# Kernel optimization log

Measured on AMD Instinct MI355X. Metric: run time of the kernel, lower is better.

Reference implementation:

```python
import jax, jax.numpy as jnp
import numpy as np

B, S, D = 2, 2048, 2048
H, KVH, HD = 32, 8, 64
GROUPS = H // KVH  # 4
NEG = -1e9


def setup_inputs() -> dict:
    key = jax.random.key(0)
    ks = jax.random.split(key, 5)
    x = jax.random.normal(ks[0], (B, S, D), dtype=jnp.float32)
    # causal additive mask [1,1,S,S]
    causal = jnp.triu(jnp.full((S, S), NEG, dtype=jnp.float32), k=1)[None, None]
    Wq = jax.random.normal(ks[1], (D, D), dtype=jnp.float32) * (D ** -0.5)
    Wk = jax.random.normal(ks[2], (KVH * HD, D), dtype=jnp.float32) * (D ** -0.5)
    Wv = jax.random.normal(ks[3], (KVH * HD, D), dtype=jnp.float32) * (D ** -0.5)
    Wo = jax.random.normal(ks[4], (D, D), dtype=jnp.float32) * (D ** -0.5)
    return {"x": x, "attention_mask": causal, "Wq": Wq, "Wk": Wk, "Wv": Wv, "Wo": Wo}


def reference(x, attention_mask, Wq, Wk, Wv, Wo):
    b, s, _ = x.shape
    # projections (nn.Linear: y = x @ W.T)
    q = (x @ Wq.T).reshape(b, s, H, HD).transpose(0, 2, 1, 3)      # [b,H,s,hd]
    k = (x @ Wk.T).reshape(b, s, KVH, HD).transpose(0, 2, 1, 3)    # [b,KVH,s,hd]
    v = (x @ Wv.T).reshape(b, s, KVH, HD).transpose(0, 2, 1, 3)
    new_kv_cache = (k, v)
    # repeat_interleave over head dim for GQA
    k = jnp.repeat(k, GROUPS, axis=1)  # [b,H,s,hd]
    v = jnp.repeat(v, GROUPS, axis=1)
    scale = 1.0 / jnp.sqrt(jnp.float32(HD))
    scores = jnp.einsum('bhqd,bhkd->bhqk', q, k) * scale
    scores = scores + attention_mask
    attn = jax.nn.softmax(scores.astype(jnp.float32), axis=-1).astype(q.dtype)
    out = jnp.einsum('bhqk,bhkd->bhqd', attn, v)  # [b,H,s,hd]
    out = out.transpose(0, 2, 1, 3).reshape(b, s, H * HD)
    output = out @ Wo.T
    return (output, new_kv_cache[0], new_kv_cache[1])
```

## Files before the change

### kernel.cpp

```cpp
#include <hip/hip_runtime.h>
#include <hip/hip_bf16.h>
#include <stdint.h>

#define B_ 2
#define S_ 2048
#define D_ 2048
#define H_ 32
#define KVH_ 8
#define HD_ 64

typedef __bf16 bf16x8 __attribute__((ext_vector_type(8)));
typedef float f32x4 __attribute__((ext_vector_type(4)));

#define MFMA16(a, b, c) __builtin_amdgcn_mfma_f32_16x16x32_bf16((a), (b), (c), 0, 0, 0)

typedef __attribute__((address_space(1))) void gvoid_t;
typedef __attribute__((address_space(3))) void lvoid_t;

__device__ __forceinline__ void async_ld16(__hip_bfloat16* lds, const __hip_bfloat16* g) {
  __builtin_amdgcn_global_load_lds((gvoid_t*)(void*)(g), (lvoid_t*)(lds), 16, 0, 0);
}

__device__ __forceinline__ unsigned short f2bu(float f) {
  __hip_bfloat16 h = __float2bfloat16(f);
  return *reinterpret_cast<unsigned short*>(&h);
}

__global__ void cast_bf16_kernel(const float* __restrict__ in,
                                 unsigned short* __restrict__ out, int n4) {
  int i = blockIdx.x * blockDim.x + threadIdx.x;
  if (i >= n4) return;
  float4 v = reinterpret_cast<const float4*>(in)[i];
  ushort4 o;
  o.x = f2bu(v.x); o.y = f2bu(v.y); o.z = f2bu(v.z); o.w = f2bu(v.w);
  reinterpret_cast<ushort4*>(out)[i] = o;
}

template <int MODE>
__global__ __launch_bounds__(256, 2)
void gemm_bt(const __hip_bfloat16* __restrict__ A,
             const __hip_bfloat16* __restrict__ W,
             float* __restrict__ Cf, __hip_bfloat16* __restrict__ Cb,
             float* __restrict__ Cf2, __hip_bfloat16* __restrict__ Cb2,
             __hip_bfloat16* __restrict__ Cb3,
             int M, int N, int K) {
  __shared__ __align__(16) __hip_bfloat16 sA[128 * 32];
  __shared__ __align__(16) __hip_bfloat16 sB[128 * 32];
  const int tid = threadIdx.x;
  const int lane = tid & 63;
  const int wv = tid >> 6;
  const int l15 = lane & 15, l4 = lane >> 4;
  const int bm = blockIdx.x * 128, bn = blockIdx.y * 128;
  const int wm = (wv >> 1) * 64, wn = (wv & 1) * 64;

  const int ci0 = tid, ci1 = tid + 256;
  const __hip_bfloat16* gA0 = A + (size_t)(bm + (ci0 >> 2)) * K + (ci0 & 3) * 8;
  const __hip_bfloat16* gA1 = A + (size_t)(bm + (ci1 >> 2)) * K + (ci1 & 3) * 8;
  const __hip_bfloat16* gB0 = W + (size_t)(bn + (ci0 >> 2)) * K + (ci0 & 3) * 8;
  const __hip_bfloat16* gB1 = W + (size_t)(bn + (ci1 >> 2)) * K + (ci1 & 3) * 8;
  __hip_bfloat16* lA0 = &sA[ci0 * 8];
  __hip_bfloat16* lA1 = &sA[ci1 * 8];
  __hip_bfloat16* lB0 = &sB[ci0 * 8];
  __hip_bfloat16* lB1 = &sB[ci1 * 8];

  f32x4 acc[4][4];
#pragma unroll
  for (int i = 0; i < 4; ++i) {
#pragma unroll
    for (int j = 0; j < 4; ++j) acc[i][j] = f32x4{0.f, 0.f, 0.f, 0.f};
  }

  for (int k0 = 0; k0 < K; k0 += 32) {
    async_ld16(lA0, gA0 + k0);
    async_ld16(lA1, gA1 + k0);
    async_ld16(lB0, gB0 + k0);
    async_ld16(lB1, gB1 + k0);
    __syncthreads();
    bf16x8 af[4], bfr[4];
#pragma unroll
    for (int i = 0; i < 4; ++i)
      af[i] = *reinterpret_cast<const bf16x8*>(&sA[(wm + i * 16 + l15) * 32 + l4 * 8]);
#pragma unroll
    for (int j = 0; j < 4; ++j)
      bfr[j] = *reinterpret_cast<const bf16x8*>(&sB[(wn + j * 16 + l15) * 32 + l4 * 8]);
#pragma unroll
    for (int i = 0; i < 4; ++i) {
#pragma unroll
      for (int j = 0; j < 4; ++j) acc[i][j] = MFMA16(af[i], bfr[j], acc[i][j]);
    }
    __syncthreads();
  }

#pragma unroll
  for (int i = 0; i < 4; ++i) {
#pragma unroll
    for (int j = 0; j < 4; ++j) {
      const int col = bn + wn + j * 16 + l15;
#pragma unroll
      for (int r = 0; r < 4; ++r) {
        const int row = bm + wm + i * 16 + l4 * 4 + r;
        const float v = acc[i][j][r];
        if (MODE == 1) {
          Cf[(size_t)row * N + col] = v;
        } else {
          if (bn < 2048) {
            Cb[(size_t)row * 2048 + col] = __float2bfloat16(v);
          } else {
            const int bb = row >> 11, s = row & 2047;
            const int kv = col - 2048;
            if (kv < 512) {
              const int g = kv >> 6, hd = kv & 63;
              const size_t idx = ((size_t)(bb * KVH_ + g) * S_ + s) * HD_ + hd;
              Cf[idx] = v;
              Cb2[idx] = __float2bfloat16(v);
            } else {
              const int vv = kv - 512;
              const int g = vv >> 6, hd = vv & 63;
              const size_t idx = ((size_t)(bb * KVH_ + g) * S_ + s) * HD_ + hd;
              Cf2[idx] = v;
              Cb3[((size_t)(bb * KVH_ + g) * HD_ + hd) * S_ + s] = __float2bfloat16(v);
            }
          }
        }
      }
    }
  }
}

__global__ __launch_bounds__(256, 2)
void attn_fused(const __hip_bfloat16* __restrict__ Qb,
                const __hip_bfloat16* __restrict__ Kb,
                const __hip_bfloat16* __restrict__ Vtb,
                __hip_bfloat16* __restrict__ AOb) {
  __shared__ __align__(16) __hip_bfloat16 sK[2][64 * 64];
  __shared__ __align__(16) __hip_bfloat16 sV[2][64 * 64];
  __shared__ __align__(16) __hip_bfloat16 sP[4 * 2 * 32 * 64];

  const int tid = threadIdx.x;
  const int lane = tid & 63;
  const int wv = tid >> 6;
  const int l15 = lane & 15, l4 = lane >> 4;
  const int qa = blockIdx.x;
  const int qb = 15 - qa;
  const int h = blockIdx.y;
  const int b = blockIdx.z;
  const int g = h >> 2;

  bf16x8 qfA[2][2], qfB[2][2];
  {
    const __hip_bfloat16* QpA =
        Qb + ((size_t)(b * S_ + qa * 128 + wv * 32)) * D_ + h * HD_;
    const __hip_bfloat16* QpB =
        Qb + ((size_t)(b * S_ + qb * 128 + wv * 32)) * D_ + h * HD_;
#pragma unroll
    for (int i = 0; i < 2; ++i) {
#pragma unroll
      for (int c = 0; c < 2; ++c) {
        qfA[i][c] = *reinterpret_cast<const bf16x8*>(
            QpA + (size_t)(i * 16 + l15) * D_ + c * 32 + l4 * 8);
        qfB[i][c] = *reinterpret_cast<const bf16x8*>(
            QpB + (size_t)(i * 16 + l15) * D_ + c * 32 + l4 * 8);
      }
    }
  }

  f32x4 oaccA[2][4], oaccB[2][4];
  f32x4 laccA[2], laccB[2];
#pragma unroll
  for (int i = 0; i < 2; ++i) {
    laccA[i] = f32x4{0.f, 0.f, 0.f, 0.f};
    laccB[i] = f32x4{0.f, 0.f, 0.f, 0.f};
#pragma unroll
    for (int j = 0; j < 4; ++j) {
      oaccA[i][j] = f32x4{0.f, 0.f, 0.f, 0.f};
      oaccB[i][j] = f32x4{0.f, 0.f, 0.f, 0.f};
    }
  }

  bf16x8 vone;
#pragma unroll
  for (int j = 0; j < 8; ++j) vone[j] = (__bf16)1.0f;

  const __hip_bfloat16* Kp = Kb + (size_t)(b * KVH_ + g) * S_ * HD_;
  const __hip_bfloat16* Vp = Vtb + (size_t)(b * KVH_ + g) * HD_ * S_;
  __hip_bfloat16* sPwB = sP + (wv * 2 + 0) * (32 * 64);
  __hip_bfloat16* sPwA = sP + (wv * 2 + 1) * (32 * 64);
  const float CE = 0.125f * 1.4426950408889634f;
  const float MSUB = 8.0f;

  const int p0 = tid, p1 = tid + 256;
  const int r0 = p0 >> 3, c0 = (p0 & 7) ^ (r0 & 7);
  const int r1 = p1 >> 3, c1 = (p1 & 7) ^ (r1 & 7);
  const __hip_bfloat16* gk0 = Kp + (size_t)r0 * HD_ + c0 * 8;
  const __hip_bfloat16* gk1 = Kp + (size_t)r1 * HD_ + c1 * 8;
  const __hip_bfloat16* gv0 = Vp + (size_t)r0 * S_ + c0 * 8;
  const __hip_bfloat16* gv1 = Vp + (size_t)r1 * S_ + c1 * 8;

  auto stage = [&](int buf) {
    async_ld16(&sK[buf][p0 * 8], gk0);
    async_ld16(&sK[buf][p1 * 8], gk1);
    async_ld16(&sV[buf][p0 * 8], gv0);
    async_ld16(&sV[buf][p1 * 8], gv1);
    gk0 += 64 * HD_; gk1 += 64 * HD_;
    gv0 += 64;       gv1 += 64;
  };

  auto pack = [&](f32x4 (&sc)[2][4], int koff, __hip_bfloat16* dst) {
    if (koff >= 0) {
#pragma unroll
      for (int i = 0; i < 2; ++i) {
#pragma unroll
        for (int jn = 0; jn < 4; ++jn) {
          const int kp = koff + jn * 16 + l15;
#pragma unroll
          for (int r = 0; r < 4; ++r) {
            const int qp = wv * 32 + i * 16 + l4 * 4 + r;
            if (kp > qp) sc[i][jn][r] = -3.0e38f;
          }
        }
      }
    }
#pragma unroll
    for (int i = 0; i < 2; ++i) {
#pragma unroll
      for (int jj = 0; jj < 4; ++jj) {
#pragma unroll
        for (int r = 0; r < 4; ++r) {
          const float p = exp2f(fmaf(sc[i][jj][r], CE, -MSUB));
          dst[(i * 16 + l4 * 4 + r) * 64 + ((jj ^ l4) * 16 + l15)] =
              __float2bfloat16(p);
        }
      }
    }
  };

  const int nsteps = 2 * qb + 2;
  const int kiA_max = 2 * qa + 1;
  stage(0);
  for (int ki = 0; ki < nsteps; ++ki) {
    const int cur = ki & 1;
    __syncthreads();
    if (ki + 1 < nsteps) stage(cur ^ 1);
    const bool doA = (ki <= kiA_max);
    const int koB = ((ki >> 1) == qb) ? (ki & 1) * 64 : -1;
    const int koA = ((ki >> 1) == qa) ? (ki & 1) * 64 : -1;

    f32x4 scB[2][4], scA[2][4];
#pragma unroll
    for (int jn = 0; jn < 4; ++jn) {
      const int row = jn * 16 + l15;
      const bf16x8 k0 = *reinterpret_cast<const bf16x8*>(
          &sK[cur][(row * 8 + (l4 ^ (row & 7))) * 8]);
      const bf16x8 k1 = *reinterpret_cast<const bf16x8*>(
          &sK[cur][(row * 8 + ((4 + l4) ^ (row & 7))) * 8]);
#pragma unroll
      for (int i = 0; i < 2; ++i) {
        f32x4 t = f32x4{0.f, 0.f, 0.f, 0.f};
        t = MFMA16(qfB[i][0], k0, t);
        t = MFMA16(qfB[i][1], k1, t);
        scB[i][jn] = t;
      }
      if (doA) {
#pragma unroll
        for (int i = 0; i < 2; ++i) {
          f32x4 t = f32x4{0.f, 0.f, 0.f, 0.f};
          t = MFMA16(qfA[i][0], k0, t);
          t = MFMA16(qfA[i][1], k1, t);
          scA[i][jn] = t;
        }
      }
    }

    pack(scB, koB, sPwB);
    if (doA) pack(scA, koA, sPwA);

    const int gr = (l15 >> 2) & 3;
#pragma unroll
    for (int kc = 0; kc < 2; ++kc) {
      bf16x8 vf[4];
#pragma unroll
      for (int jn = 0; jn < 4; ++jn) {
        const int row = jn * 16 + l15;
        vf[jn] = *reinterpret_cast<const bf16x8*>(
            &sV[cur][(row * 8 + ((kc * 4 + l4) ^ (row & 7))) * 8]);
      }
      const int pcol = (((kc * 2 + (l4 >> 1)) ^ gr) * 16 + (l4 & 1) * 8);
#pragma unroll
      for (int i = 0; i < 2; ++i) {
        const bf16x8 pf = *reinterpret_cast<const bf16x8*>(
            &sPwB[(i * 16 + l15) * 64 + pcol]);
#pragma unroll
        for (int jn = 0; jn < 4; ++jn) oaccB[i][jn] = MFMA16(pf, vf[jn], oaccB[i][jn]);
        laccB[i] = MFMA16(pf, vone, laccB[i]);
      }
      if (doA) {
#pragma unroll
        for (int i = 0; i < 2; ++i) {
          const bf16x8 pf = *reinterpret_cast<const bf16x8*>(
              &sPwA[(i * 16 + l15) * 64 + pcol]);
#pragma unroll
          for (int jn = 0; jn < 4; ++jn) oaccA[i][jn] = MFMA16(pf, vf[jn], oaccA[i][jn]);
          laccA[i] = MFMA16(pf, vone, laccA[i]);
        }
      }
    }
  }

#pragma unroll
  for (int tsel = 0; tsel < 2; ++tsel) {
    const int qt = tsel ? qb : qa;
    f32x4 (&oacc)[2][4] = tsel ? oaccB : oaccA;
    f32x4 (&lacc)[2] = tsel ? laccB : laccA;
#pragma unroll
    for (int i = 0; i < 2; ++i) {
      float inv[4];
#pragma unroll
      for (int r = 0; r < 4; ++r) inv[r] = 1.0f / lacc[i][r];
#pragma unroll
      for (int jn = 0; jn < 4; ++jn) {
#pragma unroll
        for (int r = 0; r < 4; ++r) {
          const int qp = qt * 128 + wv * 32 + i * 16 + l4 * 4 + r;
          AOb[(size_t)(b * S_ + qp) * D_ + h * HD_ + jn * 16 + l15] =
              __float2bfloat16(oacc[i][jn][r] * inv[r]);
        }
      }
    }
  }
}

extern "C" void kernel_launch(void* const* d_in, const int* in_sizes, int n_in,
                              void* d_out, int out_size, void* d_ws, size_t ws_size,
                              hipStream_t stream) {
  (void)in_sizes; (void)n_in; (void)out_size; (void)ws_size;
  const float* x = (const float*)d_in[0];
  const float* Wq = (const float*)d_in[2];
  const float* Wk = (const float*)d_in[3];
  const float* Wv = (const float*)d_in[4];
  const float* Wo = (const float*)d_in[5];

  float* outO = (float*)d_out;
  float* outK = outO + (size_t)B_ * S_ * D_;
  float* outV = outK + (size_t)B_ * KVH_ * S_ * HD_;

  char* p = (char*)d_ws;
  __hip_bfloat16* xb    = (__hip_bfloat16*)p; p += (size_t)B_ * S_ * D_ * 2;
  __hip_bfloat16* Wqkvb = (__hip_bfloat16*)p; p += (size_t)3072 * D_ * 2;
  __hip_bfloat16* Wob   = (__hip_bfloat16*)p; p += (size_t)D_ * D_ * 2;
  __hip_bfloat16* Qbf   = (__hip_bfloat16*)p; p += (size_t)B_ * S_ * D_ * 2;
  __hip_bfloat16* Kbf   = (__hip_bfloat16*)p; p += (size_t)B_ * KVH_ * S_ * HD_ * 2;
  __hip_bfloat16* Vtb   = (__hip_bfloat16*)p; p += (size_t)B_ * KVH_ * S_ * HD_ * 2;
  __hip_bfloat16* AOb   = (__hip_bfloat16*)p; p += (size_t)B_ * S_ * D_ * 2;

  auto cast = [&](const float* src, __hip_bfloat16* dst, size_t n) {
    const int n4 = (int)(n / 4);
    cast_bf16_kernel<<<dim3((n4 + 255) / 256), dim3(256), 0, stream>>>(
        src, (unsigned short*)dst, n4);
  };
  cast(x, xb, (size_t)B_ * S_ * D_);
  cast(Wq, Wqkvb, (size_t)D_ * D_);
  cast(Wk, Wqkvb + (size_t)2048 * D_, (size_t)KVH_ * HD_ * D_);
  cast(Wv, Wqkvb + (size_t)2560 * D_, (size_t)KVH_ * HD_ * D_);
  cast(Wo, Wob, (size_t)D_ * D_);

  gemm_bt<4><<<dim3(32, 24), dim3(256), 0, stream>>>(
      xb, Wqkvb, outK, Qbf, outV, Kbf, Vtb, 4096, 3072, 2048);
  attn_fused<<<dim3(8, 32, 2), dim3(256), 0, stream>>>(Qbf, Kbf, Vtb, AOb);
  gemm_bt<1><<<dim3(32, 16), dim3(256), 0, stream>>>(
      AOb, Wob, outO, nullptr, nullptr, nullptr, nullptr, 4096, 2048, 2048);
}
```

Measured before the change: 329.3 us.

## Split paired causal query tiles into separate blocks and shrink P staging

The attention kernel no longer pairs a short and a long causal query tile in one block for load balance. It launches one block per 128-row query tile (twice the grid), with the longest tiles scheduled first. The softmax P tile is now written in 32-column halves per kc step into a smaller shared buffer, and launch bounds are raised to 3 blocks per CU. Register and LDS pressure drop, so occupancy can rise, but K/V are loaded again for every block and per-block work is now uneven.

```diff
diff --git a/kernel.cpp b/kernel.cpp
--- a/kernel.cpp
+++ b/kernel.cpp
@@ -127,54 +127,44 @@
   }
 }
 
-__global__ __launch_bounds__(256, 2)
+__global__ __launch_bounds__(256, 3)
 void attn_fused(const __hip_bfloat16* __restrict__ Qb,
                 const __hip_bfloat16* __restrict__ Kb,
                 const __hip_bfloat16* __restrict__ Vtb,
                 __hip_bfloat16* __restrict__ AOb) {
   __shared__ __align__(16) __hip_bfloat16 sK[2][64 * 64];
   __shared__ __align__(16) __hip_bfloat16 sV[2][64 * 64];
-  __shared__ __align__(16) __hip_bfloat16 sP[4 * 2 * 32 * 64];
+  __shared__ __align__(16) __hip_bfloat16 sP[4][32 * 32];
 
   const int tid = threadIdx.x;
   const int lane = tid & 63;
   const int wv = tid >> 6;
   const int l15 = lane & 15, l4 = lane >> 4;
-  const int qa = blockIdx.x;
-  const int qb = 15 - qa;
+  const int qi = 15 - blockIdx.x;
   const int h = blockIdx.y;
   const int b = blockIdx.z;
   const int g = h >> 2;
 
-  bf16x8 qfA[2][2], qfB[2][2];
+  bf16x8 qf[2][2];
   {
-    const __hip_bfloat16* QpA =
-        Qb + ((size_t)(b * S_ + qa * 128 + wv * 32)) * D_ + h * HD_;
-    const __hip_bfloat16* QpB =
-        Qb + ((size_t)(b * S_ + qb * 128 + wv * 32)) * D_ + h * HD_;
+    const __hip_bfloat16* Qp =
+        Qb + ((size_t)(b * S_ + qi * 128 + wv * 32)) * D_ + h * HD_;
 #pragma unroll
     for (int i = 0; i < 2; ++i) {
 #pragma unroll
-      for (int c = 0; c < 2; ++c) {
-        qfA[i][c] = *reinterpret_cast<const bf16x8*>(
-            QpA + (size_t)(i * 16 + l15) * D_ + c * 32 + l4 * 8);
-        qfB[i][c] = *reinterpret_cast<const bf16x8*>(
-            QpB + (size_t)(i * 16 + l15) * D_ + c * 32 + l4 * 8);
-      }
-    }
-  }
-
-  f32x4 oaccA[2][4], oaccB[2][4];
-  f32x4 laccA[2], laccB[2];
+      for (int c = 0; c < 2; ++c)
+        qf[i][c] = *reinterpret_cast<const bf16x8*>(
+            Qp + (size_t)(i * 16 + l15) * D_ + c * 32 + l4 * 8);
+    }
+  }
+
+  f32x4 oacc[2][4];
+  f32x4 lacc[2];
 #pragma unroll
   for (int i = 0; i < 2; ++i) {
-    laccA[i] = f32x4{0.f, 0.f, 0.f, 0.f};
-    laccB[i] = f32x4{0.f, 0.f, 0.f, 0.f};
-#pragma unroll
-    for (int j = 0; j < 4; ++j) {
-      oaccA[i][j] = f32x4{0.f, 0.f, 0.f, 0.f};
-      oaccB[i][j] = f32x4{0.f, 0.f, 0.f, 0.f};
-    }
+    lacc[i] = f32x4{0.f, 0.f, 0.f, 0.f};
+#pragma unroll
+    for (int j = 0; j < 4; ++j) oacc[i][j] = f32x4{0.f, 0.f, 0.f, 0.f};
   }
 
   bf16x8 vone;
@@ -183,8 +173,7 @@
 
   const __hip_bfloat16* Kp = Kb + (size_t)(b * KVH_ + g) * S_ * HD_;
   const __hip_bfloat16* Vp = Vtb + (size_t)(b * KVH_ + g) * HD_ * S_;
-  __hip_bfloat16* sPwB = sP + (wv * 2 + 0) * (32 * 64);
-  __hip_bfloat16* sPwA = sP + (wv * 2 + 1) * (32 * 64);
+  __hip_bfloat16* sPw = &sP[wv][0];
   const float CE = 0.125f * 1.4426950408889634f;
   const float MSUB = 8.0f;
 
@@ -205,47 +194,15 @@
     gv0 += 64;       gv1 += 64;
   };
 
-  auto pack = [&](f32x4 (&sc)[2][4], int koff, __hip_bfloat16* dst) {
-    if (koff >= 0) {
-#pragma unroll
-      for (int i = 0; i < 2; ++i) {
-#pragma unroll
-        for (int jn = 0; jn < 4; ++jn) {
-          const int kp = koff + jn * 16 + l15;
-#pragma unroll
-          for (int r = 0; r < 4; ++r) {
-            const int qp = wv * 32 + i * 16 + l4 * 4 + r;
-            if (kp > qp) sc[i][jn][r] = -3.0e38f;
-          }
-        }
-      }
-    }
-#pragma unroll
-    for (int i = 0; i < 2; ++i) {
-#pragma unroll
-      for (int jj = 0; jj < 4; ++jj) {
-#pragma unroll
-        for (int r = 0; r < 4; ++r) {
-          const float p = exp2f(fmaf(sc[i][jj][r], CE, -MSUB));
-          dst[(i * 16 + l4 * 4 + r) * 64 + ((jj ^ l4) * 16 + l15)] =
-              __float2bfloat16(p);
-        }
-      }
-    }
-  };
-
-  const int nsteps = 2 * qb + 2;
-  const int kiA_max = 2 * qa + 1;
+  const int nsteps = 2 * qi + 2;
   stage(0);
   for (int ki = 0; ki < nsteps; ++ki) {
     const int cur = ki & 1;
     __syncthreads();
     if (ki + 1 < nsteps) stage(cur ^ 1);
-    const bool doA = (ki <= kiA_max);
-    const int koB = ((ki >> 1) == qb) ? (ki & 1) * 64 : -1;
-    const int koA = ((ki >> 1) == qa) ? (ki & 1) * 64 : -1;
-
-    f32x4 scB[2][4], scA[2][4];
+    const int ko = ((ki >> 1) == qi) ? (ki & 1) * 64 : -1;
+
+    f32x4 sc[2][4];
 #pragma unroll
     for (int jn = 0; jn < 4; ++jn) {
       const int row = jn * 16 + l15;
@@ -256,27 +213,42 @@
 #pragma unroll
       for (int i = 0; i < 2; ++i) {
         f32x4 t = f32x4{0.f, 0.f, 0.f, 0.f};
-        t = MFMA16(qfB[i][0], k0, t);
-        t = MFMA16(qfB[i][1], k1, t);
-        scB[i][jn] = t;
-      }
-      if (doA) {
-#pragma unroll
-        for (int i = 0; i < 2; ++i) {
-          f32x4 t = f32x4{0.f, 0.f, 0.f, 0.f};
-          t = MFMA16(qfA[i][0], k0, t);
-          t = MFMA16(qfA[i][1], k1, t);
-          scA[i][jn] = t;
+        t = MFMA16(qf[i][0], k0, t);
+        t = MFMA16(qf[i][1], k1, t);
+        sc[i][jn] = t;
+      }
+    }
+
+    if (ko >= 0) {
+#pragma unroll
+      for (int i = 0; i < 2; ++i) {
+#pragma unroll
+        for (int jn = 0; jn < 4; ++jn) {
+          const int kp = ko + jn * 16 + l15;
+#pragma unroll
+          for (int r = 0; r < 4; ++r) {
+            const int qp = wv * 32 + i * 16 + l4 * 4 + r;
+            if (kp > qp) sc[i][jn][r] = -3.0e38f;
+          }
         }
       }
     }
 
-    pack(scB, koB, sPwB);
-    if (doA) pack(scA, koA, sPwA);
-
-    const int gr = (l15 >> 2) & 3;
+    const int pb = (l4 >> 1) ^ ((l15 >> 2) & 1);
 #pragma unroll
     for (int kc = 0; kc < 2; ++kc) {
+#pragma unroll
+      for (int i = 0; i < 2; ++i) {
+#pragma unroll
+        for (int jj = 0; jj < 2; ++jj) {
+#pragma unroll
+          for (int r = 0; r < 4; ++r) {
+            const float p = exp2f(fmaf(sc[i][kc * 2 + jj][r], CE, -MSUB));
+            sPw[(i * 16 + l4 * 4 + r) * 32 + ((jj ^ (l4 & 1)) * 16 + l15)] =
+                __float2bfloat16(p);
+          }
+        }
+      }
       bf16x8 vf[4];
 #pragma unroll
       for (int jn = 0; jn < 4; ++jn) {
@@ -284,46 +256,29 @@
         vf[jn] = *reinterpret_cast<const bf16x8*>(
             &sV[cur][(row * 8 + ((kc * 4 + l4) ^ (row & 7))) * 8]);
       }
-      const int pcol = (((kc * 2 + (l4 >> 1)) ^ gr) * 16 + (l4 & 1) * 8);
 #pragma unroll
       for (int i = 0; i < 2; ++i) {
         const bf16x8 pf = *reinterpret_cast<const bf16x8*>(
-            &sPwB[(i * 16 + l15) * 64 + pcol]);
-#pragma unroll
-        for (int jn = 0; jn < 4; ++jn) oaccB[i][jn] = MFMA16(pf, vf[jn], oaccB[i][jn]);
-        laccB[i] = MFMA16(pf, vone, laccB[i]);
-      }
-      if (doA) {
-#pragma unroll
-        for (int i = 0; i < 2; ++i) {
-          const bf16x8 pf = *reinterpret_cast<const bf16x8*>(
-              &sPwA[(i * 16 + l15) * 64 + pcol]);
-#pragma unroll
-          for (int jn = 0; jn < 4; ++jn) oaccA[i][jn] = MFMA16(pf, vf[jn], oaccA[i][jn]);
-          laccA[i] = MFMA16(pf, vone, laccA[i]);
-        }
-      }
-    }
-  }
-
-#pragma unroll
-  for (int tsel = 0; tsel < 2; ++tsel) {
-    const int qt = tsel ? qb : qa;
-    f32x4 (&oacc)[2][4] = tsel ? oaccB : oaccA;
-    f32x4 (&lacc)[2] = tsel ? laccB : laccA;
-#pragma unroll
-    for (int i = 0; i < 2; ++i) {
-      float inv[4];
-#pragma unroll
-      for (int r = 0; r < 4; ++r) inv[r] = 1.0f / lacc[i][r];
-#pragma unroll
-      for (int jn = 0; jn < 4; ++jn) {
-#pragma unroll
-        for (int r = 0; r < 4; ++r) {
-          const int qp = qt * 128 + wv * 32 + i * 16 + l4 * 4 + r;
-          AOb[(size_t)(b * S_ + qp) * D_ + h * HD_ + jn * 16 + l15] =
-              __float2bfloat16(oacc[i][jn][r] * inv[r]);
-        }
+            &sPw[(i * 16 + l15) * 32 + pb * 16 + (l4 & 1) * 8]);
+#pragma unroll
+        for (int jn = 0; jn < 4; ++jn) oacc[i][jn] = MFMA16(pf, vf[jn], oacc[i][jn]);
+        lacc[i] = MFMA16(pf, vone, lacc[i]);
+      }
+    }
+  }
+
+#pragma unroll
+  for (int i = 0; i < 2; ++i) {
+    float inv[4];
+#pragma unroll
+    for (int r = 0; r < 4; ++r) inv[r] = 1.0f / lacc[i][r];
+#pragma unroll
+    for (int jn = 0; jn < 4; ++jn) {
+#pragma unroll
+      for (int r = 0; r < 4; ++r) {
+        const int qp = qi * 128 + wv * 32 + i * 16 + l4 * 4 + r;
+        AOb[(size_t)(b * S_ + qp) * D_ + h * HD_ + jn * 16 + l15] =
+            __float2bfloat16(oacc[i][jn][r] * inv[r]);
       }
     }
   }
@@ -365,7 +320,7 @@
 
   gemm_bt<4><<<dim3(32, 24), dim3(256), 0, stream>>>(
       xb, Wqkvb, outK, Qbf, outV, Kbf, Vtb, 4096, 3072, 2048);
-  attn_fused<<<dim3(8, 32, 2), dim3(256), 0, stream>>>(Qbf, Kbf, Vtb, AOb);
+  attn_fused<<<dim3(16, 32, 2), dim3(256), 0, stream>>>(Qbf, Kbf, Vtb, AOb);
   gemm_bt<1><<<dim3(32, 16), dim3(256), 0, stream>>>(
       AOb, Wob, outO, nullptr, nullptr, nullptr, nullptr, 4096, 2048, 2048);
 }
```

Result: slower. 371.2 us (+12.7%).
